# Performance work log

Hardware: AMD Instinct MI355X
Metric: run time of the kernel (lower is better)

## Reference

```python
import jax, jax.numpy as jnp
import numpy as np

B = 8192
IN_CH = 2048
N_SUB = 8
NETWORK_COUNTS = [150, 148, 132, 136, 76, 122, 236]  # 2 * per-hemi counts
OUT_DIM = sum(NETWORK_COUNTS)  # 1000


def setup_inputs() -> dict:
    key = jax.random.key(0)
    k1, k2, k3, k4 = jax.random.split(key, 4)
    scale = 1.0 / (IN_CH ** 0.5)
    x = jax.random.normal(k1, (B, IN_CH), dtype=jnp.float32)
    subject_ids = jax.random.randint(k2, (B,), 0, N_SUB, dtype=jnp.int64)
    # Concatenation of the 7 per-network SubjectLayers weights along the output
    # dim is mathematically identical to running each head and concatenating.
    W = jax.random.normal(k3, (N_SUB, IN_CH, OUT_DIM), dtype=jnp.float32) * scale
    b = jax.random.normal(k4, (N_SUB, OUT_DIM), dtype=jnp.float32) * scale
    return {"x": x, "subject_ids": subject_ids, "W": W, "b": b}


def reference(x, subject_ids, W, b):
    # out[b, o] = sum_d x[b, d] * W[subject_ids[b], d, o] + bias[subject_ids[b], o]
    # Compute scores against all subjects then select, avoiding materializing
    # the (B, IN_CH, OUT_DIM) gathered weight tensor.
    full = jnp.einsum('bd,sdo->bso', x, W)  # (B, N_SUB, OUT_DIM)
    sel = jnp.take_along_axis(full, subject_ids[:, None, None], axis=1)[:, 0, :]
    return sel + b[subject_ids]
```

## Files before the change

### kernel.cpp

```cpp
#include <hip/hip_runtime.h>
#include <hip/hip_bf16.h>
#include <cstdint>
#include <cstddef>

#define NROWS 8192
#define KDIM  2048
#define ODIM  1000
#define NSUB  8
#define OPAD  1024

#define BM 160
#define BN 256
#define BK 64
#define MT_MAX 8
#define ASLOT (BM * BK)
#define SLOT  ((BM + BN) * BK)

typedef __attribute__((ext_vector_type(4))) float f32x4;
typedef __attribute__((ext_vector_type(8))) short short8v;
typedef __attribute__((ext_vector_type(4))) unsigned short u16x4;
typedef __attribute__((ext_vector_type(4))) int int4v;

__device__ __forceinline__ unsigned short f2bf(float f){
  unsigned u = __builtin_bit_cast(unsigned, f);
  unsigned r = (u + 0x7FFFu + ((u >> 16) & 1u)) >> 16;
  return (unsigned short)r;
}

__device__ __forceinline__ void gload16(const void* g, void* l){
  __builtin_amdgcn_global_load_lds(
      (const __attribute__((address_space(1))) void*)g,
      (__attribute__((address_space(3))) void*)l, 16, 0, 0);
}

__global__ __launch_bounds__(256) void build_perm(const int* __restrict__ sid,
                                                  int* __restrict__ counts,
                                                  int* __restrict__ offsets,
                                                  int* __restrict__ perm){
  int s = blockIdx.x;
  __shared__ int shs[NROWS];
  __shared__ int red_lt[4], red_eq[4], wsum[4];
  __shared__ int sh_base;

  int t = threadIdx.x, lane = t & 63, wv = t >> 6;

  int c_lt = 0, c_eq = 0;
  const int4v* sv = (const int4v*)sid;
  #pragma unroll
  for (int i = 0; i < NROWS / 4 / 256; i++){
    int idx = i * 256 + t;
    int4v v = sv[idx];
    *(int4v*)&shs[idx * 4] = v;
    #pragma unroll
    for (int e = 0; e < 4; e++){ c_lt += (v[e] < s); c_eq += (v[e] == s); }
  }
  #pragma unroll
  for (int d = 32; d >= 1; d >>= 1){
    c_lt += __shfl_xor(c_lt, d);
    c_eq += __shfl_xor(c_eq, d);
  }
  if (lane == 0){ red_lt[wv] = c_lt; red_eq[wv] = c_eq; }
  __syncthreads();
  if (t == 0){
    int lt = red_lt[0] + red_lt[1] + red_lt[2] + red_lt[3];
    int eq = red_eq[0] + red_eq[1] + red_eq[2] + red_eq[3];
    offsets[s] = lt;
    counts[s]  = eq;
    sh_base = lt;
  }
  __syncthreads();
  int base = sh_base;

  for (int c0 = 0; c0 < NROWS; c0 += 256){
    int v = shs[c0 + t];
    bool eq = (v == s);
    unsigned long long m = __ballot(eq);
    int rk = __popcll(m & ((1ull << lane) - 1ull));
    int wc = __popcll(m);
    if (lane == 0) wsum[wv] = wc;
    __syncthreads();
    int woff = 0;
    #pragma unroll
    for (int w = 0; w < 4; w++) if (w < wv) woff += wsum[w];
    int tot = wsum[0] + wsum[1] + wsum[2] + wsum[3];
    if (eq) perm[base + woff + rk] = c0 + t;
    base += tot;
    __syncthreads();
  }
}

__global__ __launch_bounds__(256) void prep_fused(const float* __restrict__ x,
                                                  const int* __restrict__ perm,
                                                  unsigned short* __restrict__ xs,
                                                  const float* __restrict__ W,
                                                  unsigned short* __restrict__ Wt){
  __shared__ float tile[64][65];
  int b = blockIdx.x;
  int t = threadIdx.x;
  if (b < NROWS){
    int orow = perm[b];
    const f32x4* src = (const f32x4*)(x + (size_t)orow * KDIM);
    u16x4* dst = (u16x4*)(xs + (size_t)b * KDIM);
    #pragma unroll
    for (int c = 0; c < 2; c++){
      f32x4 v = src[c * 256 + t];
      u16x4 o;
      o[0] = f2bf(v[0]); o[1] = f2bf(v[1]); o[2] = f2bf(v[2]); o[3] = f2bf(v[3]);
      dst[c * 256 + t] = o;
    }
    return;
  }
  int b2 = b - NROWS;
  int s  = b2 >> 9;
  int kt = (b2 >> 4) & 31;
  int ot = b2 & 15;
  int k0 = kt * 64, o0 = ot * 64;
  int ol = t & 63, kr = t >> 6;
  const float* src = W + ((size_t)s * KDIM + k0) * ODIM + o0;
  bool oval = (o0 + ol) < ODIM;
  #pragma unroll
  for (int it = 0; it < 16; it++){
    int k = kr * 16 + it;
    tile[k][ol] = oval ? src[(size_t)k * ODIM + ol] : 0.f;
  }
  __syncthreads();
  int kp = t & 31, orow = t >> 5;
  unsigned short* dst = Wt + ((size_t)(s * OPAD + o0)) * KDIM + k0;
  #pragma unroll
  for (int it = 0; it < 8; it++){
    int o = orow + it * 8;
    bool valid = (o0 + o) < ODIM;
    unsigned lo = valid ? (unsigned)f2bf(tile[kp * 2][o])     : 0u;
    unsigned hi = valid ? (unsigned)f2bf(tile[kp * 2 + 1][o]) : 0u;
    *(unsigned*)(dst + (size_t)o * KDIM + kp * 2) = lo | (hi << 16);
  }
}

__global__ __launch_bounds__(512, 1) void gemm_bf16(
    const unsigned short* __restrict__ xs,
    const unsigned short* __restrict__ Wt,
    const int* __restrict__ counts,
    const int* __restrict__ offsets,
    const int* __restrict__ perm,
    const float* __restrict__ bias,
    float* __restrict__ out)
{
  int b  = blockIdx.x;
  int s  = b & 7;
  int r  = b >> 3;
  int nt = r & 3;
  int mt = r >> 2;
  int cnt = counts[s];
  int loc0 = mt * BM;
  if (loc0 >= cnt) return;
  int row0 = offsets[s] + loc0;
  int cnt_loc = cnt - loc0;

  __shared__ unsigned short L[3 * SLOT];
  __shared__ int permL[BM];

  int t = threadIdx.x;
  int lane = t & 63;
  int wave = t >> 6;

  int wm = (wave >> 2) * 80;
  int wn = (wave & 3) << 6;
  int frow = lane & 15, fk = lane >> 4;
  int axor = frow & 7;

  int srck = (((lane & 7) ^ ((lane >> 3) & 7)) << 3);
  size_t gA[5]; unsigned loA[5];
  size_t gB[6]; unsigned loB[6];
  if (wave < 4){
    #pragma unroll
    for (int i = 0; i < 5; i++){
      int ca  = wave * 5 + i;
      int row = (ca << 3) + (lane >> 3);
      int ra  = row0 + row; if (ra > NROWS - 1) ra = NROWS - 1;
      gA[i]  = (size_t)ra * KDIM + srck;
      loA[i] = (unsigned)((ca << 9) + (lane << 3));
    }
    #pragma unroll
    for (int j = 0; j < 2; j++){
      int cb  = wave * 2 + j;
      int row = (cb << 3) + (lane >> 3);
      gB[j]  = ((size_t)(s * OPAD + nt * BN + row)) * KDIM + srck;
      loB[j] = (unsigned)(ASLOT + (cb << 9) + (lane << 3));
    }
  } else {
    #pragma unroll
    for (int j = 0; j < 6; j++){
      int cb  = 8 + (wave - 4) * 6 + j;
      int row = (cb << 3) + (lane >> 3);
      gB[j]  = ((size_t)(s * OPAD + nt * BN + row)) * KDIM + srck;
      loB[j] = (unsigned)(ASLOT + (cb << 9) + (lane << 3));
    }
  }

  f32x4 acc[5][4];
  #pragma unroll
  for (int i = 0; i < 5; i++)
    #pragma unroll
    for (int j = 0; j < 4; j++)
      #pragma unroll
      for (int e = 0; e < 4; e++) acc[i][j][e] = 0.f;

#define STAGE_FULL(sl, koff) do { \
    unsigned short* Ls = &L[(sl) * SLOT]; \
    if (wave < 4){ \
      gload16(xs + gA[0] + (koff), (void*)(Ls + loA[0])); \
      gload16(xs + gA[1] + (koff), (void*)(Ls + loA[1])); \
      gload16(xs + gA[2] + (koff), (void*)(Ls + loA[2])); \
      gload16(xs + gA[3] + (koff), (void*)(Ls + loA[3])); \
      gload16(xs + gA[4] + (koff), (void*)(Ls + loA[4])); \
      gload16(Wt + gB[0] + (koff), (void*)(Ls + loB[0])); \
      gload16(Wt + gB[1] + (koff), (void*)(Ls + loB[1])); \
    } else { \
      gload16(Wt + gB[0] + (koff), (void*)(Ls + loB[0])); \
      gload16(Wt + gB[1] + (koff), (void*)(Ls + loB[1])); \
      gload16(Wt + gB[2] + (koff), (void*)(Ls + loB[2])); \
      gload16(Wt + gB[3] + (koff), (void*)(Ls + loB[3])); \
      gload16(Wt + gB[4] + (koff), (void*)(Ls + loB[4])); \
      gload16(Wt + gB[5] + (koff), (void*)(Ls + loB[5])); \
    } \
  } while (0)

#define STAGE_P0(sl, koff) do { \
    unsigned short* Ls = &L[(sl) * SLOT]; \
    if (wave < 4){ \
      gload16(xs + gA[0] + (koff), (void*)(Ls + loA[0])); \
      gload16(xs + gA[1] + (koff), (void*)(Ls + loA[1])); \
      gload16(xs + gA[2] + (koff), (void*)(Ls + loA[2])); \
      gload16(xs + gA[3] + (koff), (void*)(Ls + loA[3])); \
      gload16(xs + gA[4] + (koff), (void*)(Ls + loA[4])); \
    } else { \
      gload16(Wt + gB[0] + (koff), (void*)(Ls + loB[0])); \
      gload16(Wt + gB[1] + (koff), (void*)(Ls + loB[1])); \
      gload16(Wt + gB[2] + (koff), (void*)(Ls + loB[2])); \
    } \
  } while (0)
#define STAGE_P1(sl, koff) do { \
    unsigned short* Ls = &L[(sl) * SLOT]; \
    if (wave < 4){ \
      gload16(Wt + gB[0] + (koff), (void*)(Ls + loB[0])); \
      gload16(Wt + gB[1] + (koff), (void*)(Ls + loB[1])); \
    } else { \
      gload16(Wt + gB[3] + (koff), (void*)(Ls + loB[3])); \
      gload16(Wt + gB[4] + (koff), (void*)(Ls + loB[4])); \
      gload16(Wt + gB[5] + (koff), (void*)(Ls + loB[5])); \
    } \
  } while (0)

#define VMN() do { \
    if (wave < 4) asm volatile("s_waitcnt vmcnt(7)" ::: "memory"); \
    else          asm volatile("s_waitcnt vmcnt(6)" ::: "memory"); \
    __builtin_amdgcn_sched_barrier(0); \
  } while (0)
#define VM0() do { \
    asm volatile("s_waitcnt vmcnt(0)" ::: "memory"); \
    __builtin_amdgcn_sched_barrier(0); \
  } while (0)

#define AOFF(mi, ks) (((wm + ((mi) << 4) + frow) << 6) + ((((ks) * 4 + fk) ^ axor) << 3))
#define BOFF(ni, ks) (ASLOT + ((wn + ((ni) << 4) + frow) << 6) + ((((ks) * 4 + fk) ^ axor) << 3))
#define MF(mi, ni, av, bv) acc[mi][ni] = __builtin_amdgcn_mfma_f32_16x16x32_bf16(av, bv, acc[mi][ni], 0, 0, 0)

#define PH(sl, ks, STG, ENDW) do { \
    const unsigned short* Lb = &L[(sl) * SLOT]; \
    short8v a0 = *(const short8v*)&Lb[AOFF(0, ks)]; \
    short8v a1 = *(const short8v*)&Lb[AOFF(1, ks)]; \
    short8v a2 = *(const short8v*)&Lb[AOFF(2, ks)]; \
    short8v a3 = *(const short8v*)&Lb[AOFF(3, ks)]; \
    short8v a4 = *(const short8v*)&Lb[AOFF(4, ks)]; \
    short8v b0 = *(const short8v*)&Lb[BOFF(0, ks)]; \
    short8v b1 = *(const short8v*)&Lb[BOFF(1, ks)]; \
    short8v b2 = *(const short8v*)&Lb[BOFF(2, ks)]; \
    short8v b3 = *(const short8v*)&Lb[BOFF(3, ks)]; \
    STG; \
    __builtin_amdgcn_s_barrier(); \
    asm volatile("s_waitcnt lgkmcnt(0)" ::: "memory"); \
    __builtin_amdgcn_sched_barrier(0); \
    __builtin_amdgcn_s_setprio(1); \
    MF(0, 0, a0, b0); MF(1, 0, a1, b0); MF(2, 0, a2, b0); MF(3, 0, a3, b0); MF(4, 0, a4, b0); \
    MF(0, 1, a0, b1); MF(1, 1, a1, b1); MF(2, 1, a2, b1); MF(3, 1, a3, b1); MF(4, 1, a4, b1); \
    MF(0, 2, a0, b2); MF(1, 2, a1, b2); MF(2, 2, a2, b2); MF(3, 2, a3, b2); MF(4, 2, a4, b2); \
    MF(0, 3, a0, b3); MF(1, 3, a1, b3); MF(2, 3, a2, b3); MF(3, 3, a3, b3); MF(4, 3, a4, b3); \
    __builtin_amdgcn_s_setprio(0); \
    ENDW; \
    __builtin_amdgcn_s_barrier(); \
  } while (0)

  {
    int pr = t;
    if (pr >= 320) pr -= 320;
    if (pr >= 160) pr -= 160;
    int pidx = row0 + pr; if (pidx > NROWS - 1) pidx = NROWS - 1;
    int pl = perm[pidx];
    asm volatile("s_waitcnt vmcnt(0)" ::: "memory");
    __builtin_amdgcn_sched_barrier(0);
    permL[pr] = pl;
  }
  STAGE_FULL(0, 0);
  STAGE_FULL(1, BK);
  VMN();
  __builtin_amdgcn_s_barrier();

  for (int i = 0; i < 10; ++i){
    int kb = i * 3 * BK;
    PH(0, 0, STAGE_P0(2, kb + 2 * BK), );
    PH(0, 1, STAGE_P1(2, kb + 2 * BK), VMN());
    PH(1, 0, STAGE_P0(0, kb + 3 * BK), );
    PH(1, 1, STAGE_P1(0, kb + 3 * BK), VMN());
    PH(2, 0, STAGE_P0(1, kb + 4 * BK), );
    PH(2, 1, STAGE_P1(1, kb + 4 * BK), VMN());
  }
  PH(0, 0, , );
  PH(0, 1, , VM0());
  PH(1, 0, , );
  PH(1, 1, , );

  float bvn[4]; int ocol[4];
  #pragma unroll
  for (int ni = 0; ni < 4; ni++){
    int o = nt * BN + wn + (ni << 4) + frow;
    ocol[ni] = o;
    bvn[ni] = (o < ODIM) ? bias[s * ODIM + o] : 0.f;
  }
  #pragma unroll
  for (int mi = 0; mi < 5; mi++){
    int rbase = wm + (mi << 4) + (fk << 2);
    #pragma unroll
    for (int jj = 0; jj < 4; jj++){
      int rr = rbase + jj;
      if (rr < cnt_loc){
        int orow = permL[rr];
        #pragma unroll
        for (int ni = 0; ni < 4; ni++){
          if (ocol[ni] < ODIM)
            out[(size_t)orow * ODIM + ocol[ni]] = acc[mi][ni][jj] + bvn[ni];
        }
      }
    }
  }
#undef STAGE_FULL
#undef STAGE_P0
#undef STAGE_P1
#undef VMN
#undef VM0
#undef AOFF
#undef BOFF
#undef MF
#undef PH
}

__global__ __launch_bounds__(256) void naive_kernel(const float* __restrict__ x,
                                                    const int* __restrict__ sid,
                                                    const float* __restrict__ W,
                                                    const float* __restrict__ bias,
                                                    float* __restrict__ out){
  __shared__ float xr[KDIM];
  int row = blockIdx.x;
  int s = sid[row];
  for (int i = threadIdx.x; i < KDIM; i += 256) xr[i] = x[(size_t)row * KDIM + i];
  __syncthreads();
  int o = blockIdx.y * 256 + threadIdx.x;
  if (o >= ODIM) return;
  const float* w = W + (size_t)s * KDIM * ODIM + o;
  float acc = bias[s * ODIM + o];
  for (int k = 0; k < KDIM; k++) acc = fmaf(xr[k], w[(size_t)k * ODIM], acc);
  out[(size_t)row * ODIM + o] = acc;
}

extern "C" void kernel_launch(void* const* d_in, const int* in_sizes, int n_in,
                              void* d_out, int out_size, void* d_ws, size_t ws_size,
                              hipStream_t stream) {
  const float* x    = (const float*)d_in[0];
  const int*   sid  = (const int*)d_in[1];
  const float* W    = (const float*)d_in[2];
  const float* bias = (const float*)d_in[3];
  float* out = (float*)d_out;

  const size_t XS_BYTES = (size_t)NROWS * KDIM * 2;
  const size_t WT_BYTES = (size_t)NSUB * OPAD * KDIM * 2;
  const size_t need = 64 + (size_t)NROWS * 4 + XS_BYTES + WT_BYTES;

  if (ws_size < need){
    naive_kernel<<<dim3(NROWS, 4), 256, 0, stream>>>(x, sid, W, bias, out);
    return;
  }

  char* w = (char*)d_ws;
  int* counts  = (int*)w;
  int* offsets = counts + 8;
  int* perm    = (int*)(w + 64);
  unsigned short* xs = (unsigned short*)(w + 64 + (size_t)NROWS * 4);
  unsigned short* Wt = xs + (size_t)NROWS * KDIM;

  build_perm <<<NSUB, 256, 0, stream>>>(sid, counts, offsets, perm);
  prep_fused <<<NROWS + 4096, 256, 0, stream>>>(x, perm, xs, W, Wt);
  gemm_bf16  <<<NSUB * 4 * MT_MAX, 512, 0, stream>>>(xs, Wt, counts, offsets, perm, bias, out);
}
```

Baseline: 99.60 us.

## Move row permutation into GEMM gather and vectorize bf16 prep conversion

Result: no change. 99.61 us (+0.0%).

```diff
diff --git a/kernel.cpp b/kernel.cpp
--- a/kernel.cpp
+++ b/kernel.cpp
@@ -15,6 +15,9 @@
 #define MT_MAX 8
 #define ASLOT (BM * BK)
 #define SLOT  ((BM + BN) * BK)
+
+#define CVT_BLOCKS 2048
+#define TRN_BLOCKS 1024
 
 typedef __attribute__((ext_vector_type(4))) float f32x4;
 typedef __attribute__((ext_vector_type(8))) short short8v;
@@ -89,55 +92,74 @@
   }
 }
 
-__global__ __launch_bounds__(256) void prep_fused(const float* __restrict__ x,
-                                                  const int* __restrict__ perm,
-                                                  unsigned short* __restrict__ xs,
-                                                  const float* __restrict__ W,
-                                                  unsigned short* __restrict__ Wt){
+__global__ __launch_bounds__(256) void prep2(const float* __restrict__ x,
+                                             unsigned short* __restrict__ xb,
+                                             const float* __restrict__ W,
+                                             unsigned short* __restrict__ Wt){
   __shared__ float tile[64][65];
   int b = blockIdx.x;
   int t = threadIdx.x;
-  if (b < NROWS){
-    int orow = perm[b];
-    const f32x4* src = (const f32x4*)(x + (size_t)orow * KDIM);
-    u16x4* dst = (u16x4*)(xs + (size_t)b * KDIM);
-    #pragma unroll
-    for (int c = 0; c < 2; c++){
-      f32x4 v = src[c * 256 + t];
-      u16x4 o;
-      o[0] = f2bf(v[0]); o[1] = f2bf(v[1]); o[2] = f2bf(v[2]); o[3] = f2bf(v[3]);
-      dst[c * 256 + t] = o;
+
+  if (b < CVT_BLOCKS){
+    size_t base = (size_t)b * 8192 + (size_t)t * 8;
+    #pragma unroll
+    for (int c = 0; c < 4; c++){
+      size_t f = base + (size_t)c * 2048;
+      f32x4 v0 = *(const f32x4*)(x + f);
+      f32x4 v1 = *(const f32x4*)(x + f + 4);
+      short8v o;
+      o[0] = (short)f2bf(v0[0]); o[1] = (short)f2bf(v0[1]);
+      o[2] = (short)f2bf(v0[2]); o[3] = (short)f2bf(v0[3]);
+      o[4] = (short)f2bf(v1[0]); o[5] = (short)f2bf(v1[1]);
+      o[6] = (short)f2bf(v1[2]); o[7] = (short)f2bf(v1[3]);
+      *(short8v*)(xb + f) = o;
     }
     return;
   }
-  int b2 = b - NROWS;
-  int s  = b2 >> 9;
-  int kt = (b2 >> 4) & 31;
+
+  int b2 = b - CVT_BLOCKS;
+  int s  = b2 >> 7;
+  int kc = (b2 >> 4) & 7;
   int ot = b2 & 15;
-  int k0 = kt * 64, o0 = ot * 64;
-  int ol = t & 63, kr = t >> 6;
-  const float* src = W + ((size_t)s * KDIM + k0) * ODIM + o0;
-  bool oval = (o0 + ol) < ODIM;
-  #pragma unroll
-  for (int it = 0; it < 16; it++){
-    int k = kr * 16 + it;
-    tile[k][ol] = oval ? src[(size_t)k * ODIM + ol] : 0.f;
-  }
-  __syncthreads();
-  int kp = t & 31, orow = t >> 5;
-  unsigned short* dst = Wt + ((size_t)(s * OPAD + o0)) * KDIM + k0;
-  #pragma unroll
-  for (int it = 0; it < 8; it++){
-    int o = orow + it * 8;
-    bool valid = (o0 + o) < ODIM;
-    unsigned lo = valid ? (unsigned)f2bf(tile[kp * 2][o])     : 0u;
-    unsigned hi = valid ? (unsigned)f2bf(tile[kp * 2 + 1][o]) : 0u;
-    *(unsigned*)(dst + (size_t)o * KDIM + kp * 2) = lo | (hi << 16);
+  int o0 = ot * 64;
+
+  int kr  = t >> 4;
+  int ol4 = (t & 15) * 4;
+  bool lval = (o0 + ol4) < ODIM;
+
+  int j8   = (t & 7) * 8;
+  int orow = t >> 3;
+
+  #pragma unroll
+  for (int kk = 0; kk < 4; kk++){
+    int k0 = kc * 256 + kk * 64;
+    const float* src = W + ((size_t)s * KDIM + k0) * ODIM + o0;
+    #pragma unroll
+    for (int it = 0; it < 4; it++){
+      int k = kr + it * 16;
+      f32x4 v = lval ? *(const f32x4*)(src + (size_t)k * ODIM + ol4)
+                     : f32x4{0.f, 0.f, 0.f, 0.f};
+      tile[k][ol4 + 0] = v[0]; tile[k][ol4 + 1] = v[1];
+      tile[k][ol4 + 2] = v[2]; tile[k][ol4 + 3] = v[3];
+    }
+    __syncthreads();
+    unsigned short* dst = Wt + ((size_t)(s * OPAD + o0)) * KDIM + k0;
+    #pragma unroll
+    for (int it = 0; it < 2; it++){
+      int o = orow + it * 32;
+      bool oval = (o0 + o) < ODIM;
+      short8v w;
+      #pragma unroll
+      for (int j = 0; j < 8; j++)
+        w[j] = oval ? (short)f2bf(tile[j8 + j][o]) : (short)0;
+      *(short8v*)(dst + (size_t)o * KDIM + j8) = w;
+    }
+    __syncthreads();
   }
 }
 
 __global__ __launch_bounds__(512, 1) void gemm_bf16(
-    const unsigned short* __restrict__ xs,
+    const unsigned short* __restrict__ xb,
     const unsigned short* __restrict__ Wt,
     const int* __restrict__ counts,
     const int* __restrict__ offsets,
@@ -169,15 +191,34 @@
   int axor = frow & 7;
 
   int srck = (((lane & 7) ^ ((lane >> 3) & 7)) << 3);
+
+  int prow[5];
+  if (wave < 4){
+    #pragma unroll
+    for (int i = 0; i < 5; i++){
+      int row = ((wave * 5 + i) << 3) + (lane >> 3);
+      int pidx = row0 + row; if (pidx > NROWS - 1) pidx = NROWS - 1;
+      prow[i] = perm[pidx];
+    }
+  }
+  {
+    int pr = t;
+    if (pr >= 320) pr -= 320;
+    if (pr >= 160) pr -= 160;
+    int pidx = row0 + pr; if (pidx > NROWS - 1) pidx = NROWS - 1;
+    int pl = perm[pidx];
+    asm volatile("s_waitcnt vmcnt(0)" ::: "memory");
+    __builtin_amdgcn_sched_barrier(0);
+    permL[pr] = pl;
+  }
+
   size_t gA[5]; unsigned loA[5];
   size_t gB[6]; unsigned loB[6];
   if (wave < 4){
     #pragma unroll
     for (int i = 0; i < 5; i++){
-      int ca  = wave * 5 + i;
-      int row = (ca << 3) + (lane >> 3);
-      int ra  = row0 + row; if (ra > NROWS - 1) ra = NROWS - 1;
-      gA[i]  = (size_t)ra * KDIM + srck;
+      int ca = wave * 5 + i;
+      gA[i]  = (size_t)prow[i] * KDIM + srck;
       loA[i] = (unsigned)((ca << 9) + (lane << 3));
     }
     #pragma unroll
@@ -208,11 +249,11 @@
 #define STAGE_FULL(sl, koff) do { \
     unsigned short* Ls = &L[(sl) * SLOT]; \
     if (wave < 4){ \
-      gload16(xs + gA[0] + (koff), (void*)(Ls + loA[0])); \
-      gload16(xs + gA[1] + (koff), (void*)(Ls + loA[1])); \
-      gload16(xs + gA[2] + (koff), (void*)(Ls + loA[2])); \
-      gload16(xs + gA[3] + (koff), (void*)(Ls + loA[3])); \
-      gload16(xs + gA[4] + (koff), (void*)(Ls + loA[4])); \
+      gload16(xb + gA[0] + (koff), (void*)(Ls + loA[0])); \
+      gload16(xb + gA[1] + (koff), (void*)(Ls + loA[1])); \
+      gload16(xb + gA[2] + (koff), (void*)(Ls + loA[2])); \
+      gload16(xb + gA[3] + (koff), (void*)(Ls + loA[3])); \
+      gload16(xb + gA[4] + (koff), (void*)(Ls + loA[4])); \
       gload16(Wt + gB[0] + (koff), (void*)(Ls + loB[0])); \
       gload16(Wt + gB[1] + (koff), (void*)(Ls + loB[1])); \
     } else { \
@@ -228,11 +269,11 @@
 #define STAGE_P0(sl, koff) do { \
     unsigned short* Ls = &L[(sl) * SLOT]; \
     if (wave < 4){ \
-      gload16(xs + gA[0] + (koff), (void*)(Ls + loA[0])); \
-      gload16(xs + gA[1] + (koff), (void*)(Ls + loA[1])); \
-      gload16(xs + gA[2] + (koff), (void*)(Ls + loA[2])); \
-      gload16(xs + gA[3] + (koff), (void*)(Ls + loA[3])); \
-      gload16(xs + gA[4] + (koff), (void*)(Ls + loA[4])); \
+      gload16(xb + gA[0] + (koff), (void*)(Ls + loA[0])); \
+      gload16(xb + gA[1] + (koff), (void*)(Ls + loA[1])); \
+      gload16(xb + gA[2] + (koff), (void*)(Ls + loA[2])); \
+      gload16(xb + gA[3] + (koff), (void*)(Ls + loA[3])); \
+      gload16(xb + gA[4] + (koff), (void*)(Ls + loA[4])); \
     } else { \
       gload16(Wt + gB[0] + (koff), (void*)(Ls + loB[0])); \
       gload16(Wt + gB[1] + (koff), (void*)(Ls + loB[1])); \
@@ -290,16 +331,6 @@
     __builtin_amdgcn_s_barrier(); \
   } while (0)
 
-  {
-    int pr = t;
-    if (pr >= 320) pr -= 320;
-    if (pr >= 160) pr -= 160;
-    int pidx = row0 + pr; if (pidx > NROWS - 1) pidx = NROWS - 1;
-    int pl = perm[pidx];
-    asm volatile("s_waitcnt vmcnt(0)" ::: "memory");
-    __builtin_amdgcn_sched_barrier(0);
-    permL[pr] = pl;
-  }
   STAGE_FULL(0, 0);
   STAGE_FULL(1, BK);
   VMN();
@@ -380,9 +411,9 @@
   const float* bias = (const float*)d_in[3];
   float* out = (float*)d_out;
 
-  const size_t XS_BYTES = (size_t)NROWS * KDIM * 2;
+  const size_t XB_BYTES = (size_t)NROWS * KDIM * 2;
   const size_t WT_BYTES = (size_t)NSUB * OPAD * KDIM * 2;
-  const size_t need = 64 + (size_t)NROWS * 4 + XS_BYTES + WT_BYTES;
+  const size_t need = 64 + (size_t)NROWS * 4 + XB_BYTES + WT_BYTES;
 
   if (ws_size < need){
     naive_kernel<<<dim3(NROWS, 4), 256, 0, stream>>>(x, sid, W, bias, out);
@@ -393,10 +424,10 @@
   int* counts  = (int*)w;
   int* offsets = counts + 8;
   int* perm    = (int*)(w + 64);
-  unsigned short* xs = (unsigned short*)(w + 64 + (size_t)NROWS * 4);
-  unsigned short* Wt = xs + (size_t)NROWS * KDIM;
+  unsigned short* xb = (unsigned short*)(w + 64 + (size_t)NROWS * 4);
+  unsigned short* Wt = xb + (size_t)NROWS * KDIM;
 
   build_perm <<<NSUB, 256, 0, stream>>>(sid, counts, offsets, perm);
-  prep_fused <<<NROWS + 4096, 256, 0, stream>>>(x, perm, xs, W, Wt);
-  gemm_bf16  <<<NSUB * 4 * MT_MAX, 512, 0, stream>>>(xs, Wt, counts, offsets, perm, bias, out);
-}
+  prep2      <<<CVT_BLOCKS + TRN_BLOCKS, 256, 0, stream>>>(x, xb, W, Wt);
+  gemm_bf16  <<<NSUB * 4 * MT_MAX, 512, 0, stream>>>(xb, Wt, counts, offsets, perm, bias, out);
+}
```
